# Kernel optimization log

Hardware: AMD Instinct MI355X
Metric: run time of the kernel (lower is better)

The kernel has to match this reference:

```python
import jax, jax.numpy as jnp
import numpy as np
from jax import lax

VOCAB = 50257; IN_DIM = 1024; MEM = 1024
ATT_UNITS = 256; HOPS = 16
H1 = 1024; H2 = 512; H3 = 256; CLASSES = 5
N = 512  # maxlen == number of tree nodes (pad() is a no-op, penalty mask is zero)


def _build_tree(n):
    # Binary heap tree relabeled to DFS post-order ranks, so children always
    # have smaller rank than their parent and H accumulates in the same order
    # as the original recursive torch code.
    order = []
    def post(j):
        for c in (2 * j + 1, 2 * j + 2):
            if c < n:
                post(c)
        order.append(j)
    post(0)
    rank = {j: r for r, j in enumerate(order)}
    child_idx = np.zeros((n, 2), np.int32)
    mask = np.zeros((n, 2), np.float32)
    for j in range(n):
        r = rank[j]
        for k, c in enumerate((2 * j + 1, 2 * j + 2)):
            if c < n:
                child_idx[r, k] = rank[c]
                mask[r, k] = 1.0
    return jnp.asarray(child_idx), jnp.asarray(mask)


def setup_inputs() -> dict:
    key = jax.random.key(0)
    ks = jax.random.split(key, 24)
    def w(k, shape, s=0.05):
        return jax.random.normal(k, shape, jnp.float32) * s
    child_idx, child_mask = _build_tree(N)
    return {
        "linputs": jax.random.randint(ks[0], (N,), 0, VOCAB, jnp.int32),
        "rinputs": jax.random.randint(ks[1], (N,), 0, VOCAB, jnp.int32),
        "child_idx": child_idx,
        "child_mask": child_mask,
        "emb": w(ks[2], (VOCAB, IN_DIM)),
        "w_ioux": w(ks[3], (3 * MEM, IN_DIM)), "b_ioux": w(ks[4], (3 * MEM,)),
        "w_iouh": w(ks[5], (3 * MEM, MEM)), "b_iouh": w(ks[6], (3 * MEM,)),
        "w_fx": w(ks[7], (MEM, IN_DIM)), "b_fx": w(ks[8], (MEM,)),
        "w_fh": w(ks[9], (MEM, MEM)), "b_fh": w(ks[10], (MEM,)),
        "ws1": w(ks[11], (ATT_UNITS, MEM)),
        "ws2": w(ks[12], (HOPS, ATT_UNITS)),
        "wf": w(ks[13], (1, MEM, H1)),
        "w_lat": w(ks[14], (1, HOPS)), "b_lat": w(ks[15], (1,)),
        "w_fc": w(ks[16], (H2, 3 * H1)), "b_fc": w(ks[17], (H2,)),
        "w_out": w(ks[18], (H3, H2)), "b_out": w(ks[19], (H3,)),
        "w_out1": w(ks[20], (CLASSES, H3)), "b_out1": w(ks[21], (CLASSES,)),
    }


def _tree_lstm(x, child_idx, child_mask, w_ioux, b_ioux, w_iouh, b_iouh,
               w_fx, b_fx, w_fh, b_fh):
    # x: [N, in_dim]; nodes in post-order (children before parent).
    # Leaf case of the original (single all-zero child) is reproduced exactly
    # by masked (zero) child rows: child_h_sum = 0 and sum(f * child_c) = 0.
    n = x.shape[0]
    mem = w_fh.shape[0]
    x_iou = x @ w_ioux.T + b_ioux  # [N, 3M], precomputed input projections
    x_f = x @ w_fx.T + b_fx        # [N, M]

    def step(carry, xs):
        C, Hs = carry
        i, ci, m, xiou, xf = xs
        ch = Hs[ci] * m[:, None]   # [2, M] masked child hidden states
        cc = C[ci] * m[:, None]    # [2, M] masked child cell states
        iou = xiou + ch.sum(0) @ w_iouh.T + b_iouh
        ig, og, ug = jnp.split(iou, 3)
        ig = jax.nn.sigmoid(ig); og = jax.nn.sigmoid(og); ug = jnp.tanh(ug)
        f = jax.nn.sigmoid(ch @ w_fh.T + b_fh + xf)  # [2, M] forget per child
        c = ig * ug + (f * cc).sum(0)
        h = og * jnp.tanh(c)
        return (C.at[i].set(c), Hs.at[i].set(h)), None

    z = jnp.zeros((n, mem), x.dtype)
    (C, Hs), _ = lax.scan(step, (z, z),
                          (jnp.arange(n), child_idx, child_mask, x_iou, x_f))
    return Hs  # H stacked in DFS post-order; root hidden is Hs[-1]


def _attend(H, ws1, ws2):
    # H: [N, M]; N == maxlen so the penalty term of the original is all-zero.
    hbar = jnp.tanh(H @ ws1.T)                           # [N, att_units]
    alphas = jax.nn.softmax((hbar @ ws2.T).T, axis=-1)   # [hops, N]
    return alphas @ H, alphas[None]                      # [hops, M], [1, hops, N]


def reference(linputs, rinputs, child_idx, child_mask, emb,
              w_ioux, b_ioux, w_iouh, b_iouh, w_fx, b_fx, w_fh, b_fh,
              ws1, ws2, wf, w_lat, b_lat, w_fc, b_fc, w_out, b_out,
              w_out1, b_out1):
    tl = lambda tok: _tree_lstm(emb[tok], child_idx, child_mask,
                                w_ioux, b_ioux, w_iouh, b_iouh,
                                w_fx, b_fx, w_fh, b_fh)
    Hl = tl(linputs)
    Hr = tl(rinputs)
    Ml, attl = _attend(Hl, ws1, ws2)
    Mr, attr = _attend(Hr, ws1, ws2)
    lstate = jax.nn.relu(Ml @ wf[0])   # [hops, H1]
    rstate = jax.nn.relu(Mr @ wf[0])
    # lat_att applied on transposed matrix == left-multiply by its weight row
    lvec = w_lat @ lstate + b_lat      # [1, H1]
    rvec = w_lat @ rstate + b_lat
    fr = jnp.concatenate([jnp.abs(lvec - rvec), lvec * rvec,
                          0.5 * (lvec + rvec)], axis=1)  # [1, 3*H1]
    fc = jax.nn.leaky_relu(fr @ w_fc.T + b_fc, 0.01)
    fc2 = jax.nn.sigmoid(fc @ w_out.T + b_out)
    out = jax.nn.log_softmax(fc2 @ w_out1.T + b_out1, axis=-1)  # [1, classes]
    return out, attl, attr
```

## Files before the change

kernel.cpp:

```cpp
#include <hip/hip_runtime.h>
#include <math.h>

#define NN 512
#define MEMD 1024

typedef __attribute__((ext_vector_type(8))) short short8;
typedef __attribute__((ext_vector_type(4))) float float4v;

struct Sched {
  int child0[NN]; int child1[NN];
  float m0[NN]; float m1[NN];
  int chrow[2 * NN];
  int order[NN];
  int lvl_off[12];
};

constexpr void post_order_rec(int j, int n, int (&ord)[NN], int& cnt) {
  if (2 * j + 1 < n) post_order_rec(2 * j + 1, n, ord, cnt);
  if (2 * j + 2 < n) post_order_rec(2 * j + 2, n, ord, cnt);
  ord[cnt++] = j;
}

constexpr Sched make_sched() {
  Sched s{};
  int ord[NN] = {}; int cnt = 0;
  post_order_rec(0, NN, ord, cnt);
  int rank[NN] = {};
  for (int r = 0; r < NN; ++r) rank[ord[r]] = r;
  for (int j = 0; j < NN; ++j) {
    int r = rank[j];
    int c0 = 2 * j + 1, c1 = 2 * j + 2;
    s.child0[r] = (c0 < NN) ? rank[c0] : 0;
    s.m0[r] = (c0 < NN) ? 1.0f : 0.0f;
    s.child1[r] = (c1 < NN) ? rank[c1] : 0;
    s.m1[r] = (c1 < NN) ? 1.0f : 0.0f;
  }
  int h[NN] = {};
  for (int r = 0; r < NN; ++r) {
    int hh = 0;
    if (s.m0[r] > 0.0f) { int t = h[s.child0[r]] + 1; if (t > hh) hh = t; }
    if (s.m1[r] > 0.0f) { int t = h[s.child1[r]] + 1; if (t > hh) hh = t; }
    h[r] = hh;
  }
  int counts[12] = {};
  for (int r = 0; r < NN; ++r) counts[h[r]]++;
  s.lvl_off[0] = 0;
  for (int l = 0; l < 11; ++l) s.lvl_off[l + 1] = s.lvl_off[l] + counts[l];
  int pos[12] = {};
  for (int l = 0; l < 12; ++l) pos[l] = s.lvl_off[l];
  for (int r = 0; r < NN; ++r) s.order[pos[h[r]]++] = r;
  for (int slot = 0; slot < NN; ++slot) {
    int r = s.order[slot];
    s.chrow[2 * slot + 0] = (s.m0[r] > 0.f) ? s.child0[r] : -1;
    s.chrow[2 * slot + 1] = (s.m1[r] > 0.f) ? s.child1[r] : -1;
  }
  return s;
}

static constexpr Sched g_sched = make_sched();
__constant__ Sched c_sched = g_sched;

__device__ __forceinline__ float sigm(float x) { return 1.0f / (1.0f + expf(-x)); }

__device__ __forceinline__ unsigned short f2bf(float f) {
  union { float f; unsigned int u; } v; v.f = f;
  unsigned int r = v.u + 0x7fffu + ((v.u >> 16) & 1u);
  return (unsigned short)(r >> 16);
}

__device__ __forceinline__ void glds16(const unsigned short* g, unsigned short* l) {
  __builtin_amdgcn_global_load_lds(
      (const __attribute__((address_space(1))) void*)g,
      (__attribute__((address_space(3))) void*)l, 16, 0, 0);
}

__global__ __launch_bounds__(256) void k_cast_w(
    const float* __restrict__ w_ioux, const float* __restrict__ w_fx,
    const float* __restrict__ w_iouh, const float* __restrict__ w_fh,
    unsigned short* __restrict__ Wx, unsigned short* __restrict__ Wh)
{
  const int b = (int)blockIdx.x;
  const float* src; unsigned short* dst;
  if (b < 4096) {
    dst = Wx + (size_t)b * 1024;
    src = (b < 3072) ? w_ioux + (size_t)b * 1024 : w_fx + (size_t)(b - 3072) * 1024;
  } else {
    int r = b - 4096;
    dst = Wh + (size_t)r * 1024;
    src = (r < 3072) ? w_iouh + (size_t)r * 1024 : w_fh + (size_t)(r - 3072) * 1024;
  }
  const int t4 = threadIdx.x * 4;
  float4 v = *(const float4*)(src + t4);
  ushort4 o;
  o.x = f2bf(v.x); o.y = f2bf(v.y); o.z = f2bf(v.z); o.w = f2bf(v.w);
  *(ushort4*)(dst + t4) = o;
}

__global__ __launch_bounds__(256) void k_cast_emb(
    const int* __restrict__ lin, const int* __restrict__ rin,
    const float* __restrict__ emb, unsigned short* __restrict__ Ae)
{
  const int r = (int)blockIdx.x;
  const int tok = (r < 512) ? lin[r] : rin[r - 512];
  const float* src = emb + (size_t)tok * 1024;
  const int t4 = threadIdx.x * 4;
  float4 v = *(const float4*)(src + t4);
  ushort4 o;
  o.x = f2bf(v.x); o.y = f2bf(v.y); o.z = f2bf(v.z); o.w = f2bf(v.w);
  *(ushort4*)(Ae + (size_t)r * 1024 + t4) = o;
}

__global__ void k_zero_row(unsigned short* __restrict__ Hb) {
  unsigned int* p = (unsigned int*)(Hb + (size_t)1024 * 1024);
  p[threadIdx.x] = 0u;
  p[threadIdx.x + 256] = 0u;
}

__global__ __launch_bounds__(256) void k_gemm(
    const unsigned short* __restrict__ A, const unsigned short* __restrict__ B,
    float* __restrict__ Cout, int M, int off, int R)
{
  __shared__ unsigned short As[128 * 64];
  __shared__ unsigned short Bs[128 * 64];
  const int tid = threadIdx.x;
  const int L = tid & 63, w = tid >> 6;
  const int bx = (int)blockIdx.x, by = (int)blockIdx.y;
  const int q = (L & 7) ^ (L >> 3);

  const unsigned short* ga[4];
  const unsigned short* gb[4];
  #pragma unroll
  for (int i = 0; i < 4; ++i) {
    int c = w * 4 + i;
    int r = 8 * c + (L >> 3);
    int u = bx * 128 + r;
    int arow;
    if (off < 0) {
      arow = u;
    } else {
      if (u >= 4 * R) arow = 1024;
      else {
        int t = (u >= 2 * R) ? 1 : 0;
        int rr = u - t * 2 * R;
        int ch = c_sched.chrow[2 * (off + (rr >> 1)) + (rr & 1)];
        arow = (ch < 0) ? 1024 : t * 512 + ch;
      }
    }
    ga[i] = A + (size_t)arow * 1024 + q * 8;
    gb[i] = B + (size_t)(by * 128 + r) * 1024 + q * 8;
  }

  float4v acc[4][4];
  #pragma unroll
  for (int i = 0; i < 4; ++i)
    #pragma unroll
    for (int j = 0; j < 4; ++j) acc[i][j] = (float4v)(0.0f);

  const int wm = (w & 1) * 64, wn = (w >> 1) * 64;
  const int lr = L & 15, lq = L >> 4;

  for (int kk = 0; kk < 16; ++kk) {
    #pragma unroll
    for (int i = 0; i < 4; ++i) {
      glds16(ga[i], As + (w * 4 + i) * 512);
      glds16(gb[i], Bs + (w * 4 + i) * 512);
      ga[i] += 64; gb[i] += 64;
    }
    __syncthreads();
    #pragma unroll
    for (int kh = 0; kh < 2; ++kh) {
      short8 af[4], bf[4];
      #pragma unroll
      for (int mi = 0; mi < 4; ++mi) {
        int tr = wm + mi * 16 + lr;
        af[mi] = *(const short8*)(As + tr * 64 + (((kh * 4 + lq) ^ (tr & 7)) * 8));
      }
      #pragma unroll
      for (int ni = 0; ni < 4; ++ni) {
        int tr = wn + ni * 16 + lr;
        bf[ni] = *(const short8*)(Bs + tr * 64 + (((kh * 4 + lq) ^ (tr & 7)) * 8));
      }
      #pragma unroll
      for (int mi = 0; mi < 4; ++mi)
        #pragma unroll
        for (int ni = 0; ni < 4; ++ni)
          acc[mi][ni] = __builtin_amdgcn_mfma_f32_16x16x32_bf16(
              af[mi], bf[ni], acc[mi][ni], 0, 0, 0);
    }
    __syncthreads();
  }

  #pragma unroll
  for (int mi = 0; mi < 4; ++mi) {
    #pragma unroll
    for (int reg = 0; reg < 4; ++reg) {
      int gr = bx * 128 + wm + mi * 16 + lq * 4 + reg;
      if (gr < M) {
        #pragma unroll
        for (int ni = 0; ni < 4; ++ni) {
          int gc = by * 128 + wn + ni * 16 + lr;
          Cout[(size_t)gr * 4096 + gc] = acc[mi][ni][reg];
        }
      }
    }
  }
}

__global__ __launch_bounds__(256) void k_cell_leaf(
    const float* __restrict__ XO,
    const float* __restrict__ b_ioux, const float* __restrict__ b_iouh,
    float* __restrict__ H, float* __restrict__ C, unsigned short* __restrict__ Hb)
{
  const int s = (int)blockIdx.x;
  const int t = s >> 8, idx = s & 255;
  const int node = c_sched.order[idx];
  const size_t row = (size_t)t * 512 + node;
  for (int d = threadIdx.x; d < MEMD; d += 256) {
    float gi = XO[row * 4096 + d] + b_ioux[d] + b_iouh[d];
    float go = XO[row * 4096 + 1024 + d] + b_ioux[1024 + d] + b_iouh[1024 + d];
    float gu = XO[row * 4096 + 2048 + d] + b_ioux[2048 + d] + b_iouh[2048 + d];
    float cv = sigm(gi) * tanhf(gu);
    float hv = sigm(go) * tanhf(cv);
    C[row * MEMD + d] = cv;
    H[row * MEMD + d] = hv;
    Hb[row * MEMD + d] = f2bf(hv);
  }
}

__global__ __launch_bounds__(256) void k_cell_nl(
    const float* __restrict__ XO, const float* __restrict__ LO,
    const float* __restrict__ b_ioux, const float* __restrict__ b_iouh,
    const float* __restrict__ b_fx, const float* __restrict__ b_fh,
    float* __restrict__ H, float* __restrict__ C, unsigned short* __restrict__ Hb,
    int off, int R)
{
  const int s = (int)blockIdx.x;
  const int t = s / R, idx = s % R;
  const int node = c_sched.order[off + idx];
  const int c0 = c_sched.child0[node], c1 = c_sched.child1[node];
  const float m0 = c_sched.m0[node], m1 = c_sched.m1[node];
  const size_t row = (size_t)t * 512 + node;
  const size_t u0 = (size_t)(2 * s) * 4096;
  const size_t u1 = (size_t)(2 * s + 1) * 4096;
  for (int d = threadIdx.x; d < MEMD; d += 256) {
    float gi = XO[row * 4096 + d] + LO[u0 + d] + LO[u1 + d]
             + b_ioux[d] + b_iouh[d];
    float go = XO[row * 4096 + 1024 + d] + LO[u0 + 1024 + d] + LO[u1 + 1024 + d]
             + b_ioux[1024 + d] + b_iouh[1024 + d];
    float gu = XO[row * 4096 + 2048 + d] + LO[u0 + 2048 + d] + LO[u1 + 2048 + d]
             + b_ioux[2048 + d] + b_iouh[2048 + d];
    float xf = XO[row * 4096 + 3072 + d] + b_fx[d] + b_fh[d];
    float f0 = sigm(LO[u0 + 3072 + d] + xf);
    float f1 = sigm(LO[u1 + 3072 + d] + xf);
    float cc0 = m0 * C[((size_t)t * 512 + c0) * MEMD + d];
    float cc1 = m1 * C[((size_t)t * 512 + c1) * MEMD + d];
    float cv = sigm(gi) * tanhf(gu) + f0 * cc0 + f1 * cc1;
    float hv = sigm(go) * tanhf(cv);
    C[row * MEMD + d] = cv;
    H[row * MEMD + d] = hv;
    Hb[row * MEMD + d] = f2bf(hv);
  }
}

__global__ __launch_bounds__(256) void k_hbar(
    const float* __restrict__ H, const float* __restrict__ ws1,
    float* __restrict__ hbar)
{
  __shared__ float As2[64][17];
  __shared__ float Bs2[64][17];
  const int tid = threadIdx.x;
  const int tx = tid & 15, ty = tid >> 4;
  const int o0 = blockIdx.x * 64;
  const int r0 = blockIdx.y * 64;
  const int e = tid * 4;
  const int lm = e >> 4, lk = e & 15;
  const float* arow = H + (size_t)(r0 + lm) * MEMD;
  const float* brow = ws1 + (size_t)(o0 + lm) * MEMD;

  float acc[4][4] = {};
  for (int k0 = 0; k0 < MEMD; k0 += 16) {
    const float* pa = arow + k0 + lk;
    As2[lm][lk + 0] = pa[0]; As2[lm][lk + 1] = pa[1];
    As2[lm][lk + 2] = pa[2]; As2[lm][lk + 3] = pa[3];
    const float* pb = brow + k0 + lk;
    Bs2[lm][lk + 0] = pb[0]; Bs2[lm][lk + 1] = pb[1];
    Bs2[lm][lk + 2] = pb[2]; Bs2[lm][lk + 3] = pb[3];
    __syncthreads();
    #pragma unroll
    for (int kk = 0; kk < 16; ++kk) {
      float av[4], bv[4];
      #pragma unroll
      for (int i = 0; i < 4; ++i) av[i] = As2[ty * 4 + i][kk];
      #pragma unroll
      for (int j = 0; j < 4; ++j) bv[j] = Bs2[tx * 4 + j][kk];
      #pragma unroll
      for (int i = 0; i < 4; ++i)
        #pragma unroll
        for (int j = 0; j < 4; ++j) acc[i][j] += av[i] * bv[j];
    }
    __syncthreads();
  }
  #pragma unroll
  for (int i = 0; i < 4; ++i) {
    int r = r0 + ty * 4 + i;
    #pragma unroll
    for (int j = 0; j < 4; ++j) {
      int o = o0 + tx * 4 + j;
      hbar[(size_t)r * 256 + o] = tanhf(acc[i][j]);
    }
  }
}

__global__ __launch_bounds__(256) void k_logits(
    const float* __restrict__ hbar, const float* __restrict__ ws2,
    float* __restrict__ logits)
{
  __shared__ float hb[128][65];
  __shared__ float w2[16][256];
  const int b = (int)blockIdx.x;
  const int t = b / 4;
  const int n0 = (b % 4) * 128;
  const int tid = threadIdx.x;
  for (int e2 = tid; e2 < 16 * 256; e2 += 256) w2[e2 / 256][e2 % 256] = ws2[e2];
  const int n = tid & 127;
  const int hbase = (tid >> 7) * 8;
  float acc[8] = {};
  for (int a0 = 0; a0 < 256; a0 += 64) {
    __syncthreads();
    for (int e2 = tid; e2 < 128 * 64; e2 += 256) {
      int rr = e2 >> 6, aa = e2 & 63;
      hb[rr][aa] = hbar[(size_t)(t * 512 + n0 + rr) * 256 + a0 + aa];
    }
    __syncthreads();
    for (int aa = 0; aa < 64; ++aa) {
      float v = hb[n][aa];
      #pragma unroll
      for (int hh = 0; hh < 8; ++hh) acc[hh] += v * w2[hbase + hh][a0 + aa];
    }
  }
  #pragma unroll
  for (int hh = 0; hh < 8; ++hh)
    logits[(size_t)(t * 16 + hbase + hh) * 512 + n0 + n] = acc[hh];
}

__global__ __launch_bounds__(256) void k_softmax(
    const float* __restrict__ logits, float* __restrict__ alphas,
    float* __restrict__ out)
{
  const int b = (int)blockIdx.x;
  const int t = b / 16, h = b % 16;
  const float* lg = logits + (size_t)(t * 16 + h) * 512;
  __shared__ float red[256];
  const int tid = threadIdx.x;
  float v0 = lg[tid], v1 = lg[tid + 256];
  red[tid] = fmaxf(v0, v1);
  __syncthreads();
  for (int s2 = 128; s2 > 0; s2 >>= 1) {
    if (tid < s2) red[tid] = fmaxf(red[tid], red[tid + s2]);
    __syncthreads();
  }
  float mx = red[0];
  __syncthreads();
  float e0 = expf(v0 - mx), e1 = expf(v1 - mx);
  red[tid] = e0 + e1;
  __syncthreads();
  for (int s2 = 128; s2 > 0; s2 >>= 1) {
    if (tid < s2) red[tid] += red[tid + s2];
    __syncthreads();
  }
  float inv = 1.0f / red[0];
  float a0 = e0 * inv, a1 = e1 * inv;
  alphas[(size_t)(t * 16 + h) * 512 + tid] = a0;
  alphas[(size_t)(t * 16 + h) * 512 + tid + 256] = a1;
  out[5 + (size_t)t * 8192 + (size_t)h * 512 + tid] = a0;
  out[5 + (size_t)t * 8192 + (size_t)h * 512 + tid + 256] = a1;
}

__global__ __launch_bounds__(256) void k_attnM(
    const float* __restrict__ alphas, const float* __restrict__ H,
    float* __restrict__ M)
{
  __shared__ float al[16][512];
  const int b = (int)blockIdx.x;
  const int t = b / 4;
  const int m0 = (b % 4) * 256;
  const int tid = threadIdx.x;
  for (int e2 = tid; e2 < 16 * 512; e2 += 256)
    al[e2 >> 9][e2 & 511] = alphas[(size_t)t * 8192 + e2];
  __syncthreads();
  float acc[16] = {};
  for (int n = 0; n < 512; ++n) {
    float hv = H[((size_t)t * 512 + n) * MEMD + m0 + tid];
    #pragma unroll
    for (int h = 0; h < 16; ++h) acc[h] += al[h][n] * hv;
  }
  #pragma unroll
  for (int h = 0; h < 16; ++h)
    M[((size_t)t * 16 + h) * MEMD + m0 + tid] = acc[h];
}

__global__ __launch_bounds__(256) void k_lstate(
    const float* __restrict__ M, const float* __restrict__ wf,
    float* __restrict__ tmp)
{
  __shared__ float Ms[4][1024];
  const int b = (int)blockIdx.x;
  const int t = b / 16;
  const int rem = b % 16;
  const int h0 = (rem / 4) * 4;
  const int o0 = (rem % 4) * 256;
  const int tid = threadIdx.x;
  for (int e2 = tid; e2 < 4 * 1024; e2 += 256)
    Ms[e2 >> 10][e2 & 1023] = M[((size_t)t * 16 + h0 + (e2 >> 10)) * MEMD + (e2 & 1023)];
  __syncthreads();
  float acc[4] = {};
  for (int m = 0; m < 1024; ++m) {
    float wv = wf[(size_t)m * 1024 + o0 + tid];
    #pragma unroll
    for (int h = 0; h < 4; ++h) acc[h] += Ms[h][m] * wv;
  }
  #pragma unroll
  for (int h = 0; h < 4; ++h)
    tmp[((size_t)t * 16 + h0 + h) * 1024 + o0 + tid] = acc[h];
}

__global__ __launch_bounds__(256) void k_fr(
    const float* __restrict__ tmp,
    const float* __restrict__ w_lat, const float* __restrict__ b_lat,
    float* __restrict__ FR)
{
  __shared__ float wl[16];
  const int tid = threadIdx.x;
  if (tid < 16) wl[tid] = w_lat[tid];
  __syncthreads();
  const int o = blockIdx.x * 256 + tid;
  const float blat = b_lat[0];
  float lv = blat, rv = blat;
  #pragma unroll
  for (int h = 0; h < 16; ++h) {
    lv += wl[h] * fmaxf(tmp[(size_t)h * 1024 + o], 0.0f);
    rv += wl[h] * fmaxf(tmp[(size_t)(16 + h) * 1024 + o], 0.0f);
  }
  FR[o] = fabsf(lv - rv);
  FR[1024 + o] = lv * rv;
  FR[2048 + o] = 0.5f * (lv + rv);
}

__global__ __launch_bounds__(256) void k_fc(
    const float* __restrict__ FR, const float* __restrict__ w_fc,
    const float* __restrict__ b_fc, float* __restrict__ FC)
{
  const int j = (int)blockIdx.x;
  const int tid = threadIdx.x;
  const float* wrow = w_fc + (size_t)j * 3072;
  float acc = 0.f;
  #pragma unroll
  for (int i = 0; i < 12; ++i) {
    int k = tid + i * 256;
    acc += FR[k] * wrow[k];
  }
  __shared__ float red[256];
  red[tid] = acc;
  __syncthreads();
  for (int s2 = 128; s2 > 0; s2 >>= 1) {
    if (tid < s2) red[tid] += red[tid + s2];
    __syncthreads();
  }
  if (tid == 0) {
    float v = red[0] + b_fc[j];
    FC[j] = (v > 0.f) ? v : 0.01f * v;
  }
}

__global__ __launch_bounds__(256) void k_fc2(
    const float* __restrict__ FC, const float* __restrict__ w_out,
    const float* __restrict__ b_out, float* __restrict__ FC2)
{
  const int j = (int)blockIdx.x;
  const int tid = threadIdx.x;
  const float* wrow = w_out + (size_t)j * 512;
  float acc = FC[tid] * wrow[tid] + FC[tid + 256] * wrow[tid + 256];
  __shared__ float red[256];
  red[tid] = acc;
  __syncthreads();
  for (int s2 = 128; s2 > 0; s2 >>= 1) {
    if (tid < s2) red[tid] += red[tid + s2];
    __syncthreads();
  }
  if (tid == 0) FC2[j] = 1.0f / (1.0f + expf(-(red[0] + b_out[j])));
}

__global__ __launch_bounds__(320) void k_final(
    const float* __restrict__ FC2,
    const float* __restrict__ w_out1, const float* __restrict__ b_out1,
    float* __restrict__ out)
{
  __shared__ float lg5[5];
  const int tid = threadIdx.x;
  const int cls = tid >> 6;
  const int lane = tid & 63;
  const float* wrow = w_out1 + (size_t)cls * 256;
  float acc = 0.f;
  #pragma unroll
  for (int i = 0; i < 4; ++i) {
    int k = lane + i * 64;
    acc += FC2[k] * wrow[k];
  }
  #pragma unroll
  for (int s2 = 32; s2 > 0; s2 >>= 1) acc += __shfl_down(acc, s2, 64);
  if (lane == 0) lg5[cls] = acc + b_out1[cls];
  __syncthreads();
  if (tid == 0) {
    float mx = lg5[0];
    for (int k = 1; k < 5; ++k) mx = fmaxf(mx, lg5[k]);
    float s2 = 0.f;
    for (int k = 0; k < 5; ++k) s2 += expf(lg5[k] - mx);
    float lse = mx + logf(s2);
    for (int k = 0; k < 5; ++k) out[k] = lg5[k] - lse;
  }
}

extern "C" void kernel_launch(void* const* d_in, const int* in_sizes, int n_in,
                              void* d_out, int out_size, void* d_ws, size_t ws_size,
                              hipStream_t stream)
{
  const int*   lin    = (const int*)d_in[0];
  const int*   rin    = (const int*)d_in[1];
  const float* emb    = (const float*)d_in[4];
  const float* w_ioux = (const float*)d_in[5];
  const float* b_ioux = (const float*)d_in[6];
  const float* w_iouh = (const float*)d_in[7];
  const float* b_iouh = (const float*)d_in[8];
  const float* w_fx   = (const float*)d_in[9];
  const float* b_fx   = (const float*)d_in[10];
  const float* w_fh   = (const float*)d_in[11];
  const float* b_fh   = (const float*)d_in[12];
  const float* ws1    = (const float*)d_in[13];
  const float* ws2    = (const float*)d_in[14];
  const float* wf     = (const float*)d_in[15];
  const float* w_lat  = (const float*)d_in[16];
  const float* b_lat  = (const float*)d_in[17];
  const float* w_fc   = (const float*)d_in[18];
  const float* b_fc   = (const float*)d_in[19];
  const float* w_out  = (const float*)d_in[20];
  const float* b_out  = (const float*)d_in[21];
  const float* w_out1 = (const float*)d_in[22];
  const float* b_out1 = (const float*)d_in[23];
  float* out = (float*)d_out;

  float* fws  = (float*)d_ws;
  float* XO   = fws;
  float* LO   = XO + 1024 * 4096;
  float* H    = LO + 512 * 4096;
  float* C    = H + 1024 * 1024;
  float* HBAR = C + 1024 * 1024;
  float* LG   = HBAR + 1024 * 256;
  float* AL   = LG + 16384;
  float* MB   = AL + 16384;
  float* TMP  = MB + 32768;
  float* FR   = TMP + 32768;
  float* FC   = FR + 3072;
  float* FC2  = FC + 512;
  unsigned short* Ae = (unsigned short*)(FC2 + 256);
  unsigned short* Wx = Ae + 1024 * 1024;
  unsigned short* Wh = Wx = Wx;
  Wx = Ae + 1024 * 1024;
  Wh = Wx + 4096 * 1024;
  unsigned short* Hb = Wh + 4096 * 1024;

  k_cast_w<<<8192, 256, 0, stream>>>(w_ioux, w_fx, w_iouh, w_fh, Wx, Wh);
  k_cast_emb<<<1024, 256, 0, stream>>>(lin, rin, emb, Ae);
  k_zero_row<<<1, 256, 0, stream>>>(Hb);

  k_gemm<<<dim3(8, 32), 256, 0, stream>>>(Ae, Wx, XO, 1024, -1, 0);

  k_cell_leaf<<<512, 256, 0, stream>>>(XO, b_ioux, b_iouh, H, C, Hb);

  for (int l = 1; l < 11; ++l) {
    int off = g_sched.lvl_off[l];
    int R = g_sched.lvl_off[l + 1] - off;
    if (R <= 0) continue;
    int gx = (4 * R + 127) / 128;
    k_gemm<<<dim3(gx, 32), 256, 0, stream>>>(Hb, Wh, LO, 4 * R, off, R);
    k_cell_nl<<<2 * R, 256, 0, stream>>>(XO, LO, b_ioux, b_iouh, b_fx, b_fh,
                                         H, C, Hb, off, R);
  }

  k_hbar<<<dim3(4, 16), 256, 0, stream>>>(H, ws1, HBAR);
  k_logits<<<8, 256, 0, stream>>>(HBAR, ws2, LG);
  k_softmax<<<32, 256, 0, stream>>>(LG, AL, out);
  k_attnM<<<8, 256, 0, stream>>>(AL, H, MB);
  k_lstate<<<32, 256, 0, stream>>>(MB, wf, TMP);
  k_fr<<<4, 256, 0, stream>>>(TMP, w_lat, b_lat, FR);
  k_fc<<<512, 256, 0, stream>>>(FR, w_fc, b_fc, FC);
  k_fc2<<<256, 256, 0, stream>>>(FC, w_out, b_out, FC2);
  k_final<<<1, 320, 0, stream>>>(FC2, w_out1, b_out1, out);
}
```

Baseline: 780.2 us.

## Double-buffer and split-K the GEMM, fuse attention and tail kernels, drop launches

The bf16 MFMA GEMM now double-buffers its LDS tiles so the next K-chunk loads while the current one computes. It also gains a split-K grid dimension so the small per-level recurrent GEMMs launch more blocks, with the partial sums added up in the cell kernel. The fp32 hbar GEMM is replaced by the bf16 MFMA GEMM with 4-way split-K, and tanh plus the partial-sum reduction move into k_logits. Softmax is fused into k_attnM, fc2 and final are merged, and the zero-row kernel is folded into the embedding cast. These changes cut launch count and idle CUs in the sequential tree levels, at the cost of extra partial-sum memory traffic and lower precision for hbar.

```diff
diff --git a/kernel.cpp b/kernel.cpp
--- a/kernel.cpp
+++ b/kernel.cpp
@@ -77,17 +77,23 @@
 __global__ __launch_bounds__(256) void k_cast_w(
     const float* __restrict__ w_ioux, const float* __restrict__ w_fx,
     const float* __restrict__ w_iouh, const float* __restrict__ w_fh,
-    unsigned short* __restrict__ Wx, unsigned short* __restrict__ Wh)
+    const float* __restrict__ ws1,
+    unsigned short* __restrict__ Wx, unsigned short* __restrict__ Wh,
+    unsigned short* __restrict__ Ws1b)
 {
   const int b = (int)blockIdx.x;
   const float* src; unsigned short* dst;
   if (b < 4096) {
     dst = Wx + (size_t)b * 1024;
     src = (b < 3072) ? w_ioux + (size_t)b * 1024 : w_fx + (size_t)(b - 3072) * 1024;
-  } else {
+  } else if (b < 8192) {
     int r = b - 4096;
     dst = Wh + (size_t)r * 1024;
     src = (r < 3072) ? w_iouh + (size_t)r * 1024 : w_fh + (size_t)(r - 3072) * 1024;
+  } else {
+    int r = b - 8192;
+    dst = Ws1b + (size_t)r * 1024;
+    src = ws1 + (size_t)r * 1024;
   }
   const int t4 = threadIdx.x * 4;
   float4 v = *(const float4*)(src + t4);
@@ -98,9 +104,15 @@
 
 __global__ __launch_bounds__(256) void k_cast_emb(
     const int* __restrict__ lin, const int* __restrict__ rin,
-    const float* __restrict__ emb, unsigned short* __restrict__ Ae)
+    const float* __restrict__ emb, unsigned short* __restrict__ Ae,
+    unsigned short* __restrict__ Hb)
 {
   const int r = (int)blockIdx.x;
+  if (r == 1024) {
+    ushort4 z; z.x = 0; z.y = 0; z.z = 0; z.w = 0;
+    *(ushort4*)(Hb + (size_t)1024 * 1024 + threadIdx.x * 4) = z;
+    return;
+  }
   const int tok = (r < 512) ? lin[r] : rin[r - 512];
   const float* src = emb + (size_t)tok * 1024;
   const int t4 = threadIdx.x * 4;
@@ -110,21 +122,18 @@
   *(ushort4*)(Ae + (size_t)r * 1024 + t4) = o;
 }
 
-__global__ void k_zero_row(unsigned short* __restrict__ Hb) {
-  unsigned int* p = (unsigned int*)(Hb + (size_t)1024 * 1024);
-  p[threadIdx.x] = 0u;
-  p[threadIdx.x + 256] = 0u;
-}
-
 __global__ __launch_bounds__(256) void k_gemm(
     const unsigned short* __restrict__ A, const unsigned short* __restrict__ B,
-    float* __restrict__ Cout, int M, int off, int R)
-{
-  __shared__ unsigned short As[128 * 64];
-  __shared__ unsigned short Bs[128 * 64];
+    float* __restrict__ Cout, int M, int N, int off, int R)
+{
+  __shared__ unsigned short As[2][128 * 64];
+  __shared__ unsigned short Bs[2][128 * 64];
   const int tid = threadIdx.x;
   const int L = tid & 63, w = tid >> 6;
   const int bx = (int)blockIdx.x, by = (int)blockIdx.y;
+  const int z = (int)blockIdx.z;
+  const int nt = 16 / (int)gridDim.z;
+  const int k0 = z * nt * 64;
   const int q = (L & 7) ^ (L >> 3);
 
   const unsigned short* ga[4];
@@ -146,8 +155,8 @@
         arow = (ch < 0) ? 1024 : t * 512 + ch;
       }
     }
-    ga[i] = A + (size_t)arow * 1024 + q * 8;
-    gb[i] = B + (size_t)(by * 128 + r) * 1024 + q * 8;
+    ga[i] = A + (size_t)arow * 1024 + k0 + q * 8;
+    gb[i] = B + (size_t)(by * 128 + r) * 1024 + k0 + q * 8;
   }
 
   float4v acc[4][4];
@@ -159,26 +168,38 @@
   const int wm = (w & 1) * 64, wn = (w >> 1) * 64;
   const int lr = L & 15, lq = L >> 4;
 
-  for (int kk = 0; kk < 16; ++kk) {
-    #pragma unroll
-    for (int i = 0; i < 4; ++i) {
-      glds16(ga[i], As + (w * 4 + i) * 512);
-      glds16(gb[i], Bs + (w * 4 + i) * 512);
-      ga[i] += 64; gb[i] += 64;
-    }
-    __syncthreads();
+  #pragma unroll
+  for (int i = 0; i < 4; ++i) {
+    glds16(ga[i], &As[0][(w * 4 + i) * 512]);
+    glds16(gb[i], &Bs[0][(w * 4 + i) * 512]);
+    ga[i] += 64; gb[i] += 64;
+  }
+  __syncthreads();
+
+  int cur = 0;
+  for (int kk = 0; kk < nt; ++kk) {
+    if (kk + 1 < nt) {
+      #pragma unroll
+      for (int i = 0; i < 4; ++i) {
+        glds16(ga[i], &As[cur ^ 1][(w * 4 + i) * 512]);
+        glds16(gb[i], &Bs[cur ^ 1][(w * 4 + i) * 512]);
+        ga[i] += 64; gb[i] += 64;
+      }
+    }
+    const unsigned short* Ac = &As[cur][0];
+    const unsigned short* Bc = &Bs[cur][0];
     #pragma unroll
     for (int kh = 0; kh < 2; ++kh) {
       short8 af[4], bf[4];
       #pragma unroll
       for (int mi = 0; mi < 4; ++mi) {
         int tr = wm + mi * 16 + lr;
-        af[mi] = *(const short8*)(As + tr * 64 + (((kh * 4 + lq) ^ (tr & 7)) * 8));
+        af[mi] = *(const short8*)(Ac + tr * 64 + (((kh * 4 + lq) ^ (tr & 7)) * 8));
       }
       #pragma unroll
       for (int ni = 0; ni < 4; ++ni) {
         int tr = wn + ni * 16 + lr;
-        bf[ni] = *(const short8*)(Bs + tr * 64 + (((kh * 4 + lq) ^ (tr & 7)) * 8));
+        bf[ni] = *(const short8*)(Bc + tr * 64 + (((kh * 4 + lq) ^ (tr & 7)) * 8));
       }
       #pragma unroll
       for (int mi = 0; mi < 4; ++mi)
@@ -188,8 +209,10 @@
               af[mi], bf[ni], acc[mi][ni], 0, 0, 0);
     }
     __syncthreads();
-  }
-
+    cur ^= 1;
+  }
+
+  float* Cz = Cout + (size_t)z * M * N;
   #pragma unroll
   for (int mi = 0; mi < 4; ++mi) {
     #pragma unroll
@@ -199,11 +222,12 @@
         #pragma unroll
         for (int ni = 0; ni < 4; ++ni) {
           int gc = by * 128 + wn + ni * 16 + lr;
-          Cout[(size_t)gr * 4096 + gc] = acc[mi][ni][reg];
+          Cout[(size_t)z * M * N + (size_t)gr * N + gc] = acc[mi][ni][reg];
         }
       }
     }
   }
+  (void)Cz;
 }
 
 __global__ __launch_bounds__(256) void k_cell_leaf(
@@ -232,7 +256,7 @@
     const float* __restrict__ b_ioux, const float* __restrict__ b_iouh,
     const float* __restrict__ b_fx, const float* __restrict__ b_fh,
     float* __restrict__ H, float* __restrict__ C, unsigned short* __restrict__ Hb,
-    int off, int R)
+    int off, int R, int kz)
 {
   const int s = (int)blockIdx.x;
   const int t = s / R, idx = s % R;
@@ -242,16 +266,23 @@
   const size_t row = (size_t)t * 512 + node;
   const size_t u0 = (size_t)(2 * s) * 4096;
   const size_t u1 = (size_t)(2 * s + 1) * 4096;
+  const size_t lslab = (size_t)(4 * R) * 4096;
   for (int d = threadIdx.x; d < MEMD; d += 256) {
-    float gi = XO[row * 4096 + d] + LO[u0 + d] + LO[u1 + d]
-             + b_ioux[d] + b_iouh[d];
-    float go = XO[row * 4096 + 1024 + d] + LO[u0 + 1024 + d] + LO[u1 + 1024 + d]
-             + b_ioux[1024 + d] + b_iouh[1024 + d];
-    float gu = XO[row * 4096 + 2048 + d] + LO[u0 + 2048 + d] + LO[u1 + 2048 + d]
-             + b_ioux[2048 + d] + b_iouh[2048 + d];
+    float l_i = 0.f, l_o = 0.f, l_u = 0.f, l_f0 = 0.f, l_f1 = 0.f;
+    for (int zz = 0; zz < kz; ++zz) {
+      const float* Lz = LO + (size_t)zz * lslab;
+      l_i  += Lz[u0 + d]        + Lz[u1 + d];
+      l_o  += Lz[u0 + 1024 + d] + Lz[u1 + 1024 + d];
+      l_u  += Lz[u0 + 2048 + d] + Lz[u1 + 2048 + d];
+      l_f0 += Lz[u0 + 3072 + d];
+      l_f1 += Lz[u1 + 3072 + d];
+    }
+    float gi = XO[row * 4096 + d] + l_i + b_ioux[d] + b_iouh[d];
+    float go = XO[row * 4096 + 1024 + d] + l_o + b_ioux[1024 + d] + b_iouh[1024 + d];
+    float gu = XO[row * 4096 + 2048 + d] + l_u + b_ioux[2048 + d] + b_iouh[2048 + d];
     float xf = XO[row * 4096 + 3072 + d] + b_fx[d] + b_fh[d];
-    float f0 = sigm(LO[u0 + 3072 + d] + xf);
-    float f1 = sigm(LO[u1 + 3072 + d] + xf);
+    float f0 = sigm(l_f0 + xf);
+    float f1 = sigm(l_f1 + xf);
     float cc0 = m0 * C[((size_t)t * 512 + c0) * MEMD + d];
     float cc1 = m1 * C[((size_t)t * 512 + c1) * MEMD + d];
     float cv = sigm(gi) * tanhf(gu) + f0 * cc0 + f1 * cc1;
@@ -262,57 +293,8 @@
   }
 }
 
-__global__ __launch_bounds__(256) void k_hbar(
-    const float* __restrict__ H, const float* __restrict__ ws1,
-    float* __restrict__ hbar)
-{
-  __shared__ float As2[64][17];
-  __shared__ float Bs2[64][17];
-  const int tid = threadIdx.x;
-  const int tx = tid & 15, ty = tid >> 4;
-  const int o0 = blockIdx.x * 64;
-  const int r0 = blockIdx.y * 64;
-  const int e = tid * 4;
-  const int lm = e >> 4, lk = e & 15;
-  const float* arow = H + (size_t)(r0 + lm) * MEMD;
-  const float* brow = ws1 + (size_t)(o0 + lm) * MEMD;
-
-  float acc[4][4] = {};
-  for (int k0 = 0; k0 < MEMD; k0 += 16) {
-    const float* pa = arow + k0 + lk;
-    As2[lm][lk + 0] = pa[0]; As2[lm][lk + 1] = pa[1];
-    As2[lm][lk + 2] = pa[2]; As2[lm][lk + 3] = pa[3];
-    const float* pb = brow + k0 + lk;
-    Bs2[lm][lk + 0] = pb[0]; Bs2[lm][lk + 1] = pb[1];
-    Bs2[lm][lk + 2] = pb[2]; Bs2[lm][lk + 3] = pb[3];
-    __syncthreads();
-    #pragma unroll
-    for (int kk = 0; kk < 16; ++kk) {
-      float av[4], bv[4];
-      #pragma unroll
-      for (int i = 0; i < 4; ++i) av[i] = As2[ty * 4 + i][kk];
-      #pragma unroll
-      for (int j = 0; j < 4; ++j) bv[j] = Bs2[tx * 4 + j][kk];
-      #pragma unroll
-      for (int i = 0; i < 4; ++i)
-        #pragma unroll
-        for (int j = 0; j < 4; ++j) acc[i][j] += av[i] * bv[j];
-    }
-    __syncthreads();
-  }
-  #pragma unroll
-  for (int i = 0; i < 4; ++i) {
-    int r = r0 + ty * 4 + i;
-    #pragma unroll
-    for (int j = 0; j < 4; ++j) {
-      int o = o0 + tx * 4 + j;
-      hbar[(size_t)r * 256 + o] = tanhf(acc[i][j]);
-    }
-  }
-}
-
 __global__ __launch_bounds__(256) void k_logits(
-    const float* __restrict__ hbar, const float* __restrict__ ws2,
+    const float* __restrict__ HBR, const float* __restrict__ ws2,
     float* __restrict__ logits)
 {
   __shared__ float hb[128][65];
@@ -329,7 +311,10 @@
     __syncthreads();
     for (int e2 = tid; e2 < 128 * 64; e2 += 256) {
       int rr = e2 >> 6, aa = e2 & 63;
-      hb[rr][aa] = hbar[(size_t)(t * 512 + n0 + rr) * 256 + a0 + aa];
+      size_t idx = (size_t)(t * 512 + n0 + rr) * 256 + a0 + aa;
+      float v = HBR[idx] + HBR[262144 + idx] + HBR[2 * 262144 + idx]
+              + HBR[3 * 262144 + idx];
+      hb[rr][aa] = tanhf(v);
     }
     __syncthreads();
     for (int aa = 0; aa < 64; ++aa) {
@@ -343,60 +328,46 @@
     logits[(size_t)(t * 16 + hbase + hh) * 512 + n0 + n] = acc[hh];
 }
 
-__global__ __launch_bounds__(256) void k_softmax(
-    const float* __restrict__ logits, float* __restrict__ alphas,
-    float* __restrict__ out)
-{
-  const int b = (int)blockIdx.x;
-  const int t = b / 16, h = b % 16;
-  const float* lg = logits + (size_t)(t * 16 + h) * 512;
-  __shared__ float red[256];
-  const int tid = threadIdx.x;
-  float v0 = lg[tid], v1 = lg[tid + 256];
-  red[tid] = fmaxf(v0, v1);
-  __syncthreads();
-  for (int s2 = 128; s2 > 0; s2 >>= 1) {
-    if (tid < s2) red[tid] = fmaxf(red[tid], red[tid + s2]);
-    __syncthreads();
-  }
-  float mx = red[0];
-  __syncthreads();
-  float e0 = expf(v0 - mx), e1 = expf(v1 - mx);
-  red[tid] = e0 + e1;
-  __syncthreads();
-  for (int s2 = 128; s2 > 0; s2 >>= 1) {
-    if (tid < s2) red[tid] += red[tid + s2];
-    __syncthreads();
-  }
-  float inv = 1.0f / red[0];
-  float a0 = e0 * inv, a1 = e1 * inv;
-  alphas[(size_t)(t * 16 + h) * 512 + tid] = a0;
-  alphas[(size_t)(t * 16 + h) * 512 + tid + 256] = a1;
-  out[5 + (size_t)t * 8192 + (size_t)h * 512 + tid] = a0;
-  out[5 + (size_t)t * 8192 + (size_t)h * 512 + tid + 256] = a1;
-}
-
 __global__ __launch_bounds__(256) void k_attnM(
-    const float* __restrict__ alphas, const float* __restrict__ H,
-    float* __restrict__ M)
+    const float* __restrict__ LG, const float* __restrict__ H,
+    float* __restrict__ M, float* __restrict__ out)
 {
   __shared__ float al[16][512];
   const int b = (int)blockIdx.x;
-  const int t = b / 4;
-  const int m0 = (b % 4) * 256;
+  const int t = b >> 2;
+  const int m0 = (b & 3) * 256;
   const int tid = threadIdx.x;
   for (int e2 = tid; e2 < 16 * 512; e2 += 256)
-    al[e2 >> 9][e2 & 511] = alphas[(size_t)t * 8192 + e2];
-  __syncthreads();
+    al[e2 >> 9][e2 & 511] = LG[(size_t)t * 8192 + e2];
+  __syncthreads();
+  const int h = tid >> 4, i = tid & 15;
+  float mx = -1e30f;
+  #pragma unroll
+  for (int j = 0; j < 32; ++j) mx = fmaxf(mx, al[h][i + 16 * j]);
+  #pragma unroll
+  for (int m2 = 8; m2 >= 1; m2 >>= 1) mx = fmaxf(mx, __shfl_xor(mx, m2, 64));
+  float ev[32]; float s = 0.f;
+  #pragma unroll
+  for (int j = 0; j < 32; ++j) { ev[j] = expf(al[h][i + 16 * j] - mx); s += ev[j]; }
+  #pragma unroll
+  for (int m2 = 8; m2 >= 1; m2 >>= 1) s += __shfl_xor(s, m2, 64);
+  float inv = 1.0f / s;
+  #pragma unroll
+  for (int j = 0; j < 32; ++j) al[h][i + 16 * j] = ev[j] * inv;
+  __syncthreads();
+  if ((b & 3) == 0) {
+    for (int e2 = tid; e2 < 8192; e2 += 256)
+      out[5 + (size_t)t * 8192 + e2] = al[e2 >> 9][e2 & 511];
+  }
   float acc[16] = {};
   for (int n = 0; n < 512; ++n) {
     float hv = H[((size_t)t * 512 + n) * MEMD + m0 + tid];
     #pragma unroll
-    for (int h = 0; h < 16; ++h) acc[h] += al[h][n] * hv;
-  }
-  #pragma unroll
-  for (int h = 0; h < 16; ++h)
-    M[((size_t)t * 16 + h) * MEMD + m0 + tid] = acc[h];
+    for (int hh = 0; hh < 16; ++hh) acc[hh] += al[hh][n] * hv;
+  }
+  #pragma unroll
+  for (int hh = 0; hh < 16; ++hh)
+    M[((size_t)t * 16 + hh) * MEMD + m0 + tid] = acc[hh];
 }
 
 __global__ __launch_bounds__(256) void k_lstate(
@@ -472,43 +443,32 @@
   }
 }
 
-__global__ __launch_bounds__(256) void k_fc2(
+__global__ __launch_bounds__(256) void k_fc2final(
     const float* __restrict__ FC, const float* __restrict__ w_out,
-    const float* __restrict__ b_out, float* __restrict__ FC2)
-{
-  const int j = (int)blockIdx.x;
-  const int tid = threadIdx.x;
-  const float* wrow = w_out + (size_t)j * 512;
-  float acc = FC[tid] * wrow[tid] + FC[tid + 256] * wrow[tid + 256];
-  __shared__ float red[256];
-  red[tid] = acc;
-  __syncthreads();
-  for (int s2 = 128; s2 > 0; s2 >>= 1) {
-    if (tid < s2) red[tid] += red[tid + s2];
-    __syncthreads();
-  }
-  if (tid == 0) FC2[j] = 1.0f / (1.0f + expf(-(red[0] + b_out[j])));
-}
-
-__global__ __launch_bounds__(320) void k_final(
-    const float* __restrict__ FC2,
-    const float* __restrict__ w_out1, const float* __restrict__ b_out1,
-    float* __restrict__ out)
-{
+    const float* __restrict__ b_out, const float* __restrict__ w_out1,
+    const float* __restrict__ b_out1, float* __restrict__ out)
+{
+  __shared__ float sh[256];
   __shared__ float lg5[5];
   const int tid = threadIdx.x;
-  const int cls = tid >> 6;
-  const int lane = tid & 63;
-  const float* wrow = w_out1 + (size_t)cls * 256;
+  const float* wrow = w_out + (size_t)tid * 512;
   float acc = 0.f;
-  #pragma unroll
-  for (int i = 0; i < 4; ++i) {
-    int k = lane + i * 64;
-    acc += FC2[k] * wrow[k];
-  }
-  #pragma unroll
-  for (int s2 = 32; s2 > 0; s2 >>= 1) acc += __shfl_down(acc, s2, 64);
-  if (lane == 0) lg5[cls] = acc + b_out1[cls];
+  #pragma unroll 8
+  for (int k = 0; k < 512; ++k) acc += FC[k] * wrow[k];
+  sh[tid] = 1.0f / (1.0f + expf(-(acc + b_out[tid])));
+  __syncthreads();
+  if (tid < 160) {
+    const int cls = tid >> 5, lane = tid & 31;
+    float a = 0.f;
+    #pragma unroll
+    for (int j = 0; j < 8; ++j) {
+      int k = lane + 32 * j;
+      a += sh[k] * w_out1[(size_t)cls * 256 + k];
+    }
+    #pragma unroll
+    for (int m2 = 16; m2 >= 1; m2 >>= 1) a += __shfl_xor(a, m2, 64);
+    if (lane == 0) lg5[cls] = a + b_out1[cls];
+  }
   __syncthreads();
   if (tid == 0) {
     float mx = lg5[0];
@@ -551,28 +511,24 @@
   float* fws  = (float*)d_ws;
   float* XO   = fws;
   float* LO   = XO + 1024 * 4096;
-  float* H    = LO + 512 * 4096;
+  float* H    = LO + 1024 * 4096;
   float* C    = H + 1024 * 1024;
-  float* HBAR = C + 1024 * 1024;
-  float* LG   = HBAR + 1024 * 256;
-  float* AL   = LG + 16384;
-  float* MB   = AL + 16384;
+  float* HBR  = C + 1024 * 1024;
+  float* LG   = HBR + 4 * 1024 * 256;
+  float* MB   = LG + 16384;
   float* TMP  = MB + 32768;
   float* FR   = TMP + 32768;
   float* FC   = FR + 3072;
-  float* FC2  = FC + 512;
-  unsigned short* Ae = (unsigned short*)(FC2 + 256);
-  unsigned short* Wx = Ae + 1024 * 1024;
-  unsigned short* Wh = Wx = Wx;
-  Wx = Ae + 1024 * 1024;
-  Wh = Wx + 4096 * 1024;
-  unsigned short* Hb = Wh + 4096 * 1024;
-
-  k_cast_w<<<8192, 256, 0, stream>>>(w_ioux, w_fx, w_iouh, w_fh, Wx, Wh);
-  k_cast_emb<<<1024, 256, 0, stream>>>(lin, rin, emb, Ae);
-  k_zero_row<<<1, 256, 0, stream>>>(Hb);
-
-  k_gemm<<<dim3(8, 32), 256, 0, stream>>>(Ae, Wx, XO, 1024, -1, 0);
+  unsigned short* Ae   = (unsigned short*)(FC + 512);
+  unsigned short* Wx   = Ae + 1024 * 1024;
+  unsigned short* Wh   = Wx + 4096 * 1024;
+  unsigned short* Hb   = Wh + 4096 * 1024;
+  unsigned short* Ws1b = Hb + 1025 * 1024;
+
+  k_cast_w<<<8448, 256, 0, stream>>>(w_ioux, w_fx, w_iouh, w_fh, ws1, Wx, Wh, Ws1b);
+  k_cast_emb<<<1025, 256, 0, stream>>>(lin, rin, emb, Ae, Hb);
+
+  k_gemm<<<dim3(8, 32, 1), 256, 0, stream>>>(Ae, Wx, XO, 1024, 4096, -1, 0);
 
   k_cell_leaf<<<512, 256, 0, stream>>>(XO, b_ioux, b_iouh, H, C, Hb);
 
@@ -580,19 +536,20 @@
     int off = g_sched.lvl_off[l];
     int R = g_sched.lvl_off[l + 1] - off;
     if (R <= 0) continue;
-    int gx = (4 * R + 127) / 128;
-    k_gemm<<<dim3(gx, 32), 256, 0, stream>>>(Hb, Wh, LO, 4 * R, off, R);
+    int M4 = 4 * R;
+    int gx = (M4 + 127) / 128;
+    int kz = (M4 <= 128) ? 4 : 2;
+    k_gemm<<<dim3(gx, 32, kz), 256, 0, stream>>>(Hb, Wh, LO, M4, 4096, off, R);
     k_cell_nl<<<2 * R, 256, 0, stream>>>(XO, LO, b_ioux, b_iouh, b_fx, b_fh,
-                                         H, C, Hb, off, R);
-  }
-
-  k_hbar<<<dim3(4, 16), 256, 0, stream>>>(H, ws1, HBAR);
-  k_logits<<<8, 256, 0, stream>>>(HBAR, ws2, LG);
-  k_softmax<<<32, 256, 0, stream>>>(LG, AL, out);
-  k_attnM<<<8, 256, 0, stream>>>(AL, H, MB);
+                                         H, C, Hb, off, R, kz);
+  }
+
+  k_gemm<<<dim3(8, 2, 4), 256, 0, stream>>>(Hb, Ws1b, HBR, 1024, 256, -1, 0);
+
+  k_logits<<<8, 256, 0, stream>>>(HBR, ws2, LG);
+  k_attnM<<<8, 256, 0, stream>>>(LG, H, MB, out);
   k_lstate<<<32, 256, 0, stream>>>(MB, wf, TMP);
   k_fr<<<4, 256, 0, stream>>>(TMP, w_lat, b_lat, FR);
   k_fc<<<512, 256, 0, stream>>>(FR, w_fc, b_fc, FC);
-  k_fc2<<<256, 256, 0, stream>>>(FC, w_out, b_out, FC2);
-  k_final<<<1, 320, 0, stream>>>(FC2, w_out1, b_out1, out);
-}
+  k_fc2final<<<1, 256, 0, stream>>>(FC, w_out, b_out, w_out1, b_out1, out);
+}
```

Measured after the change: 728.4 us. 1.07x faster.
